# Optimization experiments

Hardware: AMD Instinct MI355X
Metric: run time of the kernel (lower is better)

The kernel has to match this reference:

```python
import jax, jax.numpy as jnp
import numpy as np

B, N, D, K = 16, 512, 256, 12  # batch, nodes, node_dim, num edge types (4 arg + 4 arg' + punct +/- + no_edges +/-)
ITERATION_STEPS = 1


def setup_inputs() -> dict:
    key = jax.random.key(0)
    ks = jax.random.split(key, 8)
    node = jax.random.normal(ks[0], (B, N, D), dtype=jnp.float32)
    node_mask = jax.random.randint(ks[1], (B, N), 0, 2, dtype=jnp.int32)
    graphs = jax.random.randint(ks[2], (K, B, N, N), 0, 2, dtype=jnp.int32)
    s = 1.0 / np.sqrt(D)
    Ww = jax.random.normal(ks[3], (1, D), dtype=jnp.float32) * s   # _node_weight_fc
    bw = jnp.zeros((1,), dtype=jnp.float32)
    Ws = jax.random.normal(ks[4], (D, D), dtype=jnp.float32) * s   # _self_node_fc
    bs = jnp.zeros((D,), dtype=jnp.float32)
    Wk = jax.random.normal(ks[5], (K, D, D), dtype=jnp.float32) * s  # 12 bias-free per-edge-type linears
    return {"node": node, "Ww": Ww, "bw": bw, "Ws": Ws, "bs": bs, "Wk": Wk,
            "node_mask": node_mask, "graphs": graphs}


def reference(node, Ww, bw, Ws, bs, Wk, node_mask, graphs):
    dt = node.dtype
    mask = node_mask.astype(dt)
    eye = jnp.eye(N, dtype=dt)
    # dd_graph = mask_row * mask_col * (1 - diag)
    dd = mask[:, None, :] * mask[:, :, None] * (1.0 - eye)          # [B,N,N]
    g = dd[None] * graphs.astype(dt)                                # [K,B,N,N] masked adjacencies
    neigh = g.sum(axis=(0, 3))                                      # [B,N] total neighbor count
    neigh = jnp.where(neigh >= 1, neigh, jnp.ones((), dt))

    all_w = []
    for _ in range(ITERATION_STEPS):
        # (1) node relatedness
        w = jax.nn.sigmoid(node @ Ww.T + bw)[..., 0]                # [B,N]
        all_w.append(w)
        self_info = node @ Ws.T + bs                                # [B,N,D]
        # (2) message propagation for all 12 edge types, batched
        trans = jnp.einsum('bnd,ked->kbne', node, Wk)               # [K,B,N,D] per-type linear (x @ W.T)
        wg = w[None, :, None, :] * g                                # [K,B,N,N] masked node weights
        agg = jnp.einsum('kbmn,kbnd->bmd', wg, trans) / neigh[..., None]
        # (3) update
        node = jax.nn.relu(self_info + agg)

    all_weight = jnp.stack(all_w, axis=1)                           # [B,steps,N]
    return node, all_weight
```

## Files before the change

### kernel.cpp

```cpp
#include <hip/hip_runtime.h>
#include <hip/hip_bf16.h>
#include <math.h>

#define BB 16
#define NN 512
#define DD 256
#define KK 12

typedef __bf16 bf16x8 __attribute__((ext_vector_type(8)));
typedef __bf16 bf16x4 __attribute__((ext_vector_type(4)));
typedef float  f32x4  __attribute__((ext_vector_type(4)));

#define WS_WM     0
#define WS_MASKBF 32768
#define WS_NODEBF 49152
#define WS_NODET  4243456
#define WS_WKBF   8437760
#define WS_WSBF   10010624

__global__ __launch_bounds__(256) void k1_prep(const float* __restrict__ node,
        const float* __restrict__ Ww, const float* __restrict__ bw,
        const int* __restrict__ node_mask,
        float* __restrict__ wm, __bf16* __restrict__ maskbf,
        __bf16* __restrict__ node_bf, float* __restrict__ all_w) {
    int t = threadIdx.x;
    int lane = t & 63;
    int row = blockIdx.x * 4 + (t >> 6);
    const float4 nv = *(const float4*)(node + (size_t)row * DD + lane * 4);
    const float4 wv = *(const float4*)(Ww + lane * 4);
    float dot = nv.x*wv.x + nv.y*wv.y + nv.z*wv.z + nv.w*wv.w;
    #pragma unroll
    for (int off = 32; off > 0; off >>= 1) dot += __shfl_xor(dot, off);
    float w = 1.0f / (1.0f + expf(-(dot + bw[0])));
    int mk = node_mask[row];
    if (lane == 0) {
        wm[row]     = w * (float)mk;
        all_w[row]  = w;
        maskbf[row] = (__bf16)(float)mk;
    }
    bf16x4 nb = {(__bf16)nv.x, (__bf16)nv.y, (__bf16)nv.z, (__bf16)nv.w};
    *(bf16x4*)(node_bf + (size_t)row * DD + lane * 4) = nb;
}

__global__ __launch_bounds__(256) void k1b_convert(const float* __restrict__ Wk,
        const float* __restrict__ Ws, __bf16* __restrict__ Wk_bf, __bf16* __restrict__ Ws_bf) {
    const int KDD = KK * DD * DD;
    int idx = (blockIdx.x * 256 + threadIdx.x) * 4;
    if (idx < KDD) {
        float4 v = *(const float4*)(Wk + idx);
        bf16x4 o = {(__bf16)v.x, (__bf16)v.y, (__bf16)v.z, (__bf16)v.w};
        *(bf16x4*)(Wk_bf + idx) = o;
    } else {
        int j = idx - KDD;
        if (j < DD * DD) {
            float4 v = *(const float4*)(Ws + j);
            bf16x4 o = {(__bf16)v.x, (__bf16)v.y, (__bf16)v.z, (__bf16)v.w};
            *(bf16x4*)(Ws_bf + j) = o;
        }
    }
}

__global__ __launch_bounds__(256) void k2_transpose(const float* __restrict__ node,
        const float* __restrict__ wm, __bf16* __restrict__ dst) {
    __shared__ float tile[64][65];
    int bx = blockIdx.x;
    int b = bx >> 5; int rest = bx & 31; int nt = rest >> 2; int dt = rest & 3;
    int n0 = nt * 64, d0 = dt * 64;
    int t = threadIdx.x;
    #pragma unroll
    for (int i = 0; i < 16; i++) {
        int idx = i * 256 + t;
        int n = idx >> 6, d = idx & 63;
        tile[n][d] = node[((size_t)(b * NN + n0 + n)) * DD + d0 + d];
    }
    __syncthreads();
    #pragma unroll
    for (int i = 0; i < 16; i++) {
        int idx = i * 256 + t;
        int d = idx >> 6, n = idx & 63;
        float w = wm[b * NN + n0 + n];
        dst[((size_t)(b * DD + d0 + d)) * NN + n0 + n] = (__bf16)(tile[n][d] * w);
    }
}

__global__ __launch_bounds__(512, 2) void k45_fused(const int* __restrict__ graphs,
        const int* __restrict__ node_mask, const __bf16* __restrict__ maskbf,
        const __bf16* __restrict__ node_t, const __bf16* __restrict__ node_bf,
        const __bf16* __restrict__ Wk_bf, const __bf16* __restrict__ Ws_bf,
        const float* __restrict__ bs, float* __restrict__ out) {
    __shared__ __align__(16) __bf16 Abf[32][520];
    __shared__ __align__(16) __bf16 Tk[32][264];
    __shared__ float cntp[8][32];
    __shared__ float sm[32];
    int bx = blockIdx.x;
    int b  = (bx & 7) + 8 * ((bx >> 3) & 1);
    int mt = bx >> 4;
    int m0 = mt * 32;
    int t = threadIdx.x;
    int lane = t & 63;
    int w = t >> 6;
    int q = lane >> 4;
    int l16 = lane & 15;
    int esub = w * 32;
    int dsub = w * 32;

    int crow = t >> 7;
    int ccol = (t & 127) * 4;

    f32x4 accO[2][2];
    #pragma unroll
    for (int i = 0; i < 2; i++)
        #pragma unroll
        for (int j = 0; j < 2; j++) accO[i][j] = (f32x4){0.f, 0.f, 0.f, 0.f};
    f32x4 accC[2];
    accC[0] = (f32x4){0.f, 0.f, 0.f, 0.f};
    accC[1] = (f32x4){0.f, 0.f, 0.f, 0.f};

    int4 g[8];
    {
        const int4* gb = (const int4*)(graphs + ((size_t)(b * NN + m0)) * NN);
        #pragma unroll
        for (int u = 0; u < 8; u++) g[u] = gb[u * 512 + t];
    }

    #pragma unroll 1
    for (int k = 0; k < KK; k++) {
        #pragma unroll
        for (int u = 0; u < 8; u++) {
            int row = u * 4 + crow;
            unsigned p0 = (unsigned)g[u].x | ((unsigned)g[u].y << 16);
            unsigned p1 = (unsigned)g[u].z | ((unsigned)g[u].w << 16);
            unsigned drel = (unsigned)(m0 + row - ccol);
            if (drel < 2u)      p0 &= ~(0xFFFFu << (16 * drel));
            else if (drel < 4u) p1 &= ~(0xFFFFu << (16 * (drel - 2)));
            uint2 st; st.x = p0 * 0x3F80u; st.y = p1 * 0x3F80u;
            *(uint2*)&Abf[row][ccol] = st;
        }
        __syncthreads();

        if (k < KK - 1) {
            const int4* gb = (const int4*)(graphs + ((size_t)(((k + 1) * BB + b) * NN + m0)) * NN);
            #pragma unroll
            for (int u = 0; u < 8; u++) g[u] = gb[u * 512 + t];
        }

        f32x4 accT[2][2];
        #pragma unroll
        for (int i = 0; i < 2; i++)
            #pragma unroll
            for (int j = 0; j < 2; j++) accT[i][j] = (f32x4){0.f, 0.f, 0.f, 0.f};
        #pragma unroll
        for (int kk = 0; kk < 16; kk++) {
            int n0c = kk * 32;
            bf16x8 af[2], bfr[2];
            #pragma unroll
            for (int fm = 0; fm < 2; fm++)
                af[fm] = *(const bf16x8*)&Abf[fm * 16 + l16][n0c + q * 8];
            #pragma unroll
            for (int fd = 0; fd < 2; fd++)
                bfr[fd] = *(const bf16x8*)(node_t +
                    ((size_t)(b * DD + esub + fd * 16 + l16)) * NN + n0c + q * 8);
            #pragma unroll
            for (int fm = 0; fm < 2; fm++)
                #pragma unroll
                for (int fd = 0; fd < 2; fd++)
                    accT[fm][fd] = __builtin_amdgcn_mfma_f32_16x16x32_bf16(
                        af[fm], bfr[fd], accT[fm][fd], 0, 0, 0);
            if ((kk >> 1) == w) {
                bf16x8 bfm = (bf16x8){0,0,0,0,0,0,0,0};
                if (l16 == 0)
                    bfm = *(const bf16x8*)(maskbf + b * NN + n0c + q * 8);
                accC[0] = __builtin_amdgcn_mfma_f32_16x16x32_bf16(af[0], bfm, accC[0], 0, 0, 0);
                accC[1] = __builtin_amdgcn_mfma_f32_16x16x32_bf16(af[1], bfm, accC[1], 0, 0, 0);
            }
        }
        #pragma unroll
        for (int fm = 0; fm < 2; fm++)
            #pragma unroll
            for (int fd = 0; fd < 2; fd++) {
                int col = esub + fd * 16 + l16;
                #pragma unroll
                for (int r = 0; r < 4; r++)
                    Tk[fm * 16 + q * 4 + r][col] = (__bf16)accT[fm][fd][r];
            }
        __syncthreads();

        #pragma unroll
        for (int ee = 0; ee < 8; ee++) {
            int e0c = ee * 32;
            bf16x8 afT[2], bw2[2];
            #pragma unroll
            for (int fm = 0; fm < 2; fm++)
                afT[fm] = *(const bf16x8*)&Tk[fm * 16 + l16][e0c + q * 8];
            #pragma unroll
            for (int fd = 0; fd < 2; fd++)
                bw2[fd] = *(const bf16x8*)(Wk_bf +
                    ((size_t)(k * DD + dsub + fd * 16 + l16)) * DD + e0c + q * 8);
            #pragma unroll
            for (int fm = 0; fm < 2; fm++)
                #pragma unroll
                for (int fd = 0; fd < 2; fd++)
                    accO[fm][fd] = __builtin_amdgcn_mfma_f32_16x16x32_bf16(
                        afT[fm], bw2[fd], accO[fm][fd], 0, 0, 0);
        }
    }

    if (l16 == 0) {
        #pragma unroll
        for (int fm = 0; fm < 2; fm++)
            #pragma unroll
            for (int r = 0; r < 4; r++)
                cntp[w][fm * 16 + q * 4 + r] = accC[fm][r];
    }
    __syncthreads();
    if (t < 32) {
        float c = 0.0f;
        #pragma unroll
        for (int w8 = 0; w8 < 8; w8++) c += cntp[w8][t];
        int mk = node_mask[b * NN + m0 + t];
        sm[t] = (float)mk / (c >= 0.5f ? c : 1.0f);
    }
    __syncthreads();

    #pragma unroll
    for (int fm = 0; fm < 2; fm++)
        #pragma unroll
        for (int r = 0; r < 4; r++) {
            float s = sm[fm * 16 + q * 4 + r];
            #pragma unroll
            for (int fd = 0; fd < 2; fd++) accO[fm][fd][r] *= s;
        }

    #pragma unroll
    for (int ee = 0; ee < 8; ee++) {
        int e0c = ee * 32;
        bf16x8 afS[2], bwS[2];
        #pragma unroll
        for (int fm = 0; fm < 2; fm++)
            afS[fm] = *(const bf16x8*)(node_bf +
                ((size_t)(b * NN + m0 + fm * 16 + l16)) * DD + e0c + q * 8);
        #pragma unroll
        for (int fd = 0; fd < 2; fd++)
            bwS[fd] = *(const bf16x8*)(Ws_bf +
                ((size_t)(dsub + fd * 16 + l16)) * DD + e0c + q * 8);
        #pragma unroll
        for (int fm = 0; fm < 2; fm++)
            #pragma unroll
            for (int fd = 0; fd < 2; fd++)
                accO[fm][fd] = __builtin_amdgcn_mfma_f32_16x16x32_bf16(
                    afS[fm], bwS[fd], accO[fm][fd], 0, 0, 0);
    }

    #pragma unroll
    for (int fm = 0; fm < 2; fm++)
        #pragma unroll
        for (int fd = 0; fd < 2; fd++) {
            int d = dsub + fd * 16 + l16;
            float bsv = bs[d];
            #pragma unroll
            for (int r = 0; r < 4; r++) {
                int m = m0 + fm * 16 + q * 4 + r;
                float v = accO[fm][fd][r] + bsv;
                out[((size_t)(b * NN + m)) * DD + d] = fmaxf(v, 0.0f);
            }
        }
}

extern "C" void kernel_launch(void* const* d_in, const int* in_sizes, int n_in,
                              void* d_out, int out_size, void* d_ws, size_t ws_size,
                              hipStream_t stream) {
    const float* node      = (const float*)d_in[0];
    const float* Ww        = (const float*)d_in[1];
    const float* bw        = (const float*)d_in[2];
    const float* Ws        = (const float*)d_in[3];
    const float* bs        = (const float*)d_in[4];
    const float* Wk        = (const float*)d_in[5];
    const int*   node_mask = (const int*)d_in[6];
    const int*   graphs    = (const int*)d_in[7];
    float* out   = (float*)d_out;
    float* all_w = out + (size_t)BB * NN * DD;

    char* ws = (char*)d_ws;
    float*  wm      = (float*)(ws + WS_WM);
    __bf16* maskbf  = (__bf16*)(ws + WS_MASKBF);
    __bf16* node_bf = (__bf16*)(ws + WS_NODEBF);
    __bf16* node_t  = (__bf16*)(ws + WS_NODET);
    __bf16* Wk_bf   = (__bf16*)(ws + WS_WKBF);
    __bf16* Ws_bf   = (__bf16*)(ws + WS_WSBF);

    k1_prep    <<<2048, 256, 0, stream>>>(node, Ww, bw, node_mask, wm, maskbf, node_bf, all_w);
    k1b_convert<<< 832, 256, 0, stream>>>(Wk, Ws, Wk_bf, Ws_bf);
    k2_transpose<<<512, 256, 0, stream>>>(node, wm, node_t);
    k45_fused  <<< 256, 512, 0, stream>>>(graphs, node_mask, maskbf, node_t, node_bf,
                                          Wk_bf, Ws_bf, bs, out);
}
```

Measured before the change: 354.8 us.

## Split fused graph kernel into 16-row tiles with halved output columns per block

The fused aggregation kernel changes from 256 blocks of 512 threads, each handling 32 rows, to 1024 blocks of 256 threads. Each block now handles 16 rows and half of the output feature dimension. The intent is to spread work over more blocks and waves per CU to raise occupancy and hide latency. The cost is that each pair of blocks recomputes the full adjacency-times-node product and reads the same graph tiles twice, adding redundant MFMA work and memory traffic.

```diff
diff --git a/kernel.cpp b/kernel.cpp
--- a/kernel.cpp
+++ b/kernel.cpp
@@ -83,51 +83,48 @@
     }
 }
 
-__global__ __launch_bounds__(512, 2) void k45_fused(const int* __restrict__ graphs,
+__global__ __launch_bounds__(256, 4) void k45_fused(const int* __restrict__ graphs,
         const int* __restrict__ node_mask, const __bf16* __restrict__ maskbf,
         const __bf16* __restrict__ node_t, const __bf16* __restrict__ node_bf,
         const __bf16* __restrict__ Wk_bf, const __bf16* __restrict__ Ws_bf,
         const float* __restrict__ bs, float* __restrict__ out) {
-    __shared__ __align__(16) __bf16 Abf[32][520];
-    __shared__ __align__(16) __bf16 Tk[32][264];
-    __shared__ float cntp[8][32];
-    __shared__ float sm[32];
+    __shared__ __align__(16) __bf16 Abf[16][520];
+    __shared__ __align__(16) __bf16 Tk[16][264];
+    __shared__ float cntp[4][16];
+    __shared__ float sm[16];
     int bx = blockIdx.x;
     int b  = (bx & 7) + 8 * ((bx >> 3) & 1);
-    int mt = bx >> 4;
-    int m0 = mt * 32;
+    int dh = (bx >> 4) & 1;
+    int mt = bx >> 5;
+    int m0 = mt * 16;
     int t = threadIdx.x;
     int lane = t & 63;
     int w = t >> 6;
     int q = lane >> 4;
     int l16 = lane & 15;
-    int esub = w * 32;
-    int dsub = w * 32;
-
-    int crow = t >> 7;
-    int ccol = (t & 127) * 4;
-
-    f32x4 accO[2][2];
-    #pragma unroll
-    for (int i = 0; i < 2; i++)
-        #pragma unroll
-        for (int j = 0; j < 2; j++) accO[i][j] = (f32x4){0.f, 0.f, 0.f, 0.f};
-    f32x4 accC[2];
-    accC[0] = (f32x4){0.f, 0.f, 0.f, 0.f};
-    accC[1] = (f32x4){0.f, 0.f, 0.f, 0.f};
+    int esub = w * 64;
+    int dsub = dh * 128 + w * 32;
+
+    int rowpar = t >> 7;
+    int ccol   = (t & 127) * 4;
+
+    f32x4 accO[2];
+    accO[0] = (f32x4){0.f, 0.f, 0.f, 0.f};
+    accO[1] = (f32x4){0.f, 0.f, 0.f, 0.f};
+    f32x4 accC = (f32x4){0.f, 0.f, 0.f, 0.f};
 
     int4 g[8];
     {
         const int4* gb = (const int4*)(graphs + ((size_t)(b * NN + m0)) * NN);
         #pragma unroll
-        for (int u = 0; u < 8; u++) g[u] = gb[u * 512 + t];
+        for (int u = 0; u < 8; u++) g[u] = gb[u * 256 + t];
     }
 
     #pragma unroll 1
     for (int k = 0; k < KK; k++) {
         #pragma unroll
         for (int u = 0; u < 8; u++) {
-            int row = u * 4 + crow;
+            int row = u * 2 + rowpar;
             unsigned p0 = (unsigned)g[u].x | ((unsigned)g[u].y << 16);
             unsigned p1 = (unsigned)g[u].z | ((unsigned)g[u].w << 16);
             unsigned drel = (unsigned)(m0 + row - ccol);
@@ -141,129 +138,100 @@
         if (k < KK - 1) {
             const int4* gb = (const int4*)(graphs + ((size_t)(((k + 1) * BB + b) * NN + m0)) * NN);
             #pragma unroll
-            for (int u = 0; u < 8; u++) g[u] = gb[u * 512 + t];
-        }
-
-        f32x4 accT[2][2];
-        #pragma unroll
-        for (int i = 0; i < 2; i++)
-            #pragma unroll
-            for (int j = 0; j < 2; j++) accT[i][j] = (f32x4){0.f, 0.f, 0.f, 0.f};
+            for (int u = 0; u < 8; u++) g[u] = gb[u * 256 + t];
+        }
+
+        f32x4 accT[4];
+        #pragma unroll
+        for (int i = 0; i < 4; i++) accT[i] = (f32x4){0.f, 0.f, 0.f, 0.f};
         #pragma unroll
         for (int kk = 0; kk < 16; kk++) {
             int n0c = kk * 32;
-            bf16x8 af[2], bfr[2];
-            #pragma unroll
-            for (int fm = 0; fm < 2; fm++)
-                af[fm] = *(const bf16x8*)&Abf[fm * 16 + l16][n0c + q * 8];
-            #pragma unroll
-            for (int fd = 0; fd < 2; fd++)
+            bf16x8 af = *(const bf16x8*)&Abf[l16][n0c + q * 8];
+            bf16x8 bfr[4];
+            #pragma unroll
+            for (int fd = 0; fd < 4; fd++)
                 bfr[fd] = *(const bf16x8*)(node_t +
                     ((size_t)(b * DD + esub + fd * 16 + l16)) * NN + n0c + q * 8);
             #pragma unroll
-            for (int fm = 0; fm < 2; fm++)
-                #pragma unroll
-                for (int fd = 0; fd < 2; fd++)
-                    accT[fm][fd] = __builtin_amdgcn_mfma_f32_16x16x32_bf16(
-                        af[fm], bfr[fd], accT[fm][fd], 0, 0, 0);
-            if ((kk >> 1) == w) {
+            for (int fd = 0; fd < 4; fd++)
+                accT[fd] = __builtin_amdgcn_mfma_f32_16x16x32_bf16(af, bfr[fd], accT[fd], 0, 0, 0);
+            if ((kk >> 2) == w) {
                 bf16x8 bfm = (bf16x8){0,0,0,0,0,0,0,0};
                 if (l16 == 0)
                     bfm = *(const bf16x8*)(maskbf + b * NN + n0c + q * 8);
-                accC[0] = __builtin_amdgcn_mfma_f32_16x16x32_bf16(af[0], bfm, accC[0], 0, 0, 0);
-                accC[1] = __builtin_amdgcn_mfma_f32_16x16x32_bf16(af[1], bfm, accC[1], 0, 0, 0);
+                accC = __builtin_amdgcn_mfma_f32_16x16x32_bf16(af, bfm, accC, 0, 0, 0);
             }
         }
         #pragma unroll
-        for (int fm = 0; fm < 2; fm++)
-            #pragma unroll
-            for (int fd = 0; fd < 2; fd++) {
-                int col = esub + fd * 16 + l16;
-                #pragma unroll
-                for (int r = 0; r < 4; r++)
-                    Tk[fm * 16 + q * 4 + r][col] = (__bf16)accT[fm][fd][r];
-            }
+        for (int fd = 0; fd < 4; fd++) {
+            int col = esub + fd * 16 + l16;
+            #pragma unroll
+            for (int r = 0; r < 4; r++)
+                Tk[q * 4 + r][col] = (__bf16)accT[fd][r];
+        }
         __syncthreads();
 
         #pragma unroll
         for (int ee = 0; ee < 8; ee++) {
             int e0c = ee * 32;
-            bf16x8 afT[2], bw2[2];
-            #pragma unroll
-            for (int fm = 0; fm < 2; fm++)
-                afT[fm] = *(const bf16x8*)&Tk[fm * 16 + l16][e0c + q * 8];
+            bf16x8 afT = *(const bf16x8*)&Tk[l16][e0c + q * 8];
+            bf16x8 bw2[2];
             #pragma unroll
             for (int fd = 0; fd < 2; fd++)
                 bw2[fd] = *(const bf16x8*)(Wk_bf +
                     ((size_t)(k * DD + dsub + fd * 16 + l16)) * DD + e0c + q * 8);
             #pragma unroll
-            for (int fm = 0; fm < 2; fm++)
-                #pragma unroll
-                for (int fd = 0; fd < 2; fd++)
-                    accO[fm][fd] = __builtin_amdgcn_mfma_f32_16x16x32_bf16(
-                        afT[fm], bw2[fd], accO[fm][fd], 0, 0, 0);
+            for (int fd = 0; fd < 2; fd++)
+                accO[fd] = __builtin_amdgcn_mfma_f32_16x16x32_bf16(afT, bw2[fd], accO[fd], 0, 0, 0);
         }
     }
 
     if (l16 == 0) {
         #pragma unroll
-        for (int fm = 0; fm < 2; fm++)
-            #pragma unroll
-            for (int r = 0; r < 4; r++)
-                cntp[w][fm * 16 + q * 4 + r] = accC[fm][r];
+        for (int r = 0; r < 4; r++) cntp[w][q * 4 + r] = accC[r];
     }
     __syncthreads();
-    if (t < 32) {
-        float c = 0.0f;
-        #pragma unroll
-        for (int w8 = 0; w8 < 8; w8++) c += cntp[w8][t];
+    if (t < 16) {
+        float c = cntp[0][t] + cntp[1][t] + cntp[2][t] + cntp[3][t];
         int mk = node_mask[b * NN + m0 + t];
         sm[t] = (float)mk / (c >= 0.5f ? c : 1.0f);
     }
     __syncthreads();
 
     #pragma unroll
-    for (int fm = 0; fm < 2; fm++)
-        #pragma unroll
-        for (int r = 0; r < 4; r++) {
-            float s = sm[fm * 16 + q * 4 + r];
-            #pragma unroll
-            for (int fd = 0; fd < 2; fd++) accO[fm][fd][r] *= s;
-        }
+    for (int r = 0; r < 4; r++) {
+        float s = sm[q * 4 + r];
+        accO[0][r] *= s;
+        accO[1][r] *= s;
+    }
 
     #pragma unroll
     for (int ee = 0; ee < 8; ee++) {
         int e0c = ee * 32;
-        bf16x8 afS[2], bwS[2];
-        #pragma unroll
-        for (int fm = 0; fm < 2; fm++)
-            afS[fm] = *(const bf16x8*)(node_bf +
-                ((size_t)(b * NN + m0 + fm * 16 + l16)) * DD + e0c + q * 8);
+        bf16x8 afS = *(const bf16x8*)(node_bf +
+            ((size_t)(b * NN + m0 + l16)) * DD + e0c + q * 8);
+        bf16x8 bwS[2];
         #pragma unroll
         for (int fd = 0; fd < 2; fd++)
             bwS[fd] = *(const bf16x8*)(Ws_bf +
                 ((size_t)(dsub + fd * 16 + l16)) * DD + e0c + q * 8);
         #pragma unroll
-        for (int fm = 0; fm < 2; fm++)
-            #pragma unroll
-            for (int fd = 0; fd < 2; fd++)
-                accO[fm][fd] = __builtin_amdgcn_mfma_f32_16x16x32_bf16(
-                    afS[fm], bwS[fd], accO[fm][fd], 0, 0, 0);
-    }
-
-    #pragma unroll
-    for (int fm = 0; fm < 2; fm++)
-        #pragma unroll
-        for (int fd = 0; fd < 2; fd++) {
-            int d = dsub + fd * 16 + l16;
-            float bsv = bs[d];
-            #pragma unroll
-            for (int r = 0; r < 4; r++) {
-                int m = m0 + fm * 16 + q * 4 + r;
-                float v = accO[fm][fd][r] + bsv;
-                out[((size_t)(b * NN + m)) * DD + d] = fmaxf(v, 0.0f);
-            }
-        }
+        for (int fd = 0; fd < 2; fd++)
+            accO[fd] = __builtin_amdgcn_mfma_f32_16x16x32_bf16(afS, bwS[fd], accO[fd], 0, 0, 0);
+    }
+
+    #pragma unroll
+    for (int fd = 0; fd < 2; fd++) {
+        int d = dsub + fd * 16 + l16;
+        float bsv = bs[d];
+        #pragma unroll
+        for (int r = 0; r < 4; r++) {
+            int m = m0 + q * 4 + r;
+            float v = accO[fd][r] + bsv;
+            out[((size_t)(b * NN + m)) * DD + d] = fmaxf(v, 0.0f);
+        }
+    }
 }
 
 extern "C" void kernel_launch(void* const* d_in, const int* in_sizes, int n_in,
@@ -291,6 +259,6 @@
     k1_prep    <<<2048, 256, 0, stream>>>(node, Ww, bw, node_mask, wm, maskbf, node_bf, all_w);
     k1b_convert<<< 832, 256, 0, stream>>>(Wk, Ws, Wk_bf, Ws_bf);
     k2_transpose<<<512, 256, 0, stream>>>(node, wm, node_t);
-    k45_fused  <<< 256, 512, 0, stream>>>(graphs, node_mask, maskbf, node_t, node_bf,
+    k45_fused  <<<1024, 256, 0, stream>>>(graphs, node_mask, maskbf, node_t, node_bf,
                                           Wk_bf, Ws_bf, bs, out);
 }
```

New measurement: 928.1 us. 2.62x slower.

## Split edge-type loop across two blocks with partial sums and epilogue kernel

Applied to the files above, without the earlier changes.

The fused kernel's loop over 12 edge types is split into two halves handled by separate blocks, which doubles the grid from 256 to 512 blocks to fill more of the GPU's compute units. Each half writes fp32 partial aggregates to workspace and atomically adds neighbor counts. A new epilogue kernel sums the partials, applies the normalization, and computes the self-node linear plus bias and ReLU. The cost is an extra kernel launch, a memset, and about 16MB of extra global traffic for the partial aggregates.

```diff
diff --git a/kernel.cpp b/kernel.cpp
--- a/kernel.cpp
+++ b/kernel.cpp
@@ -12,11 +12,13 @@
 typedef float  f32x4  __attribute__((ext_vector_type(4)));
 
 #define WS_WM     0
-#define WS_MASKBF 32768
-#define WS_NODEBF 49152
-#define WS_NODET  4243456
-#define WS_WKBF   8437760
-#define WS_WSBF   10010624
+#define WS_NCNT   32768
+#define WS_MASKBF 65536
+#define WS_NODEBF 81920
+#define WS_NODET  4276224
+#define WS_WKBF   8470528
+#define WS_WSBF   10043392
+#define WS_AGG    10174464
 
 __global__ __launch_bounds__(256) void k1_prep(const float* __restrict__ node,
         const float* __restrict__ Ww, const float* __restrict__ bw,
@@ -83,18 +85,16 @@
     }
 }
 
-__global__ __launch_bounds__(512, 2) void k45_fused(const int* __restrict__ graphs,
-        const int* __restrict__ node_mask, const __bf16* __restrict__ maskbf,
-        const __bf16* __restrict__ node_t, const __bf16* __restrict__ node_bf,
-        const __bf16* __restrict__ Wk_bf, const __bf16* __restrict__ Ws_bf,
-        const float* __restrict__ bs, float* __restrict__ out) {
+__global__ __launch_bounds__(512, 2) void k45_partial(const int* __restrict__ graphs,
+        const __bf16* __restrict__ maskbf, const __bf16* __restrict__ node_t,
+        const __bf16* __restrict__ Wk_bf, float* __restrict__ Agg, int* __restrict__ ncnt) {
     __shared__ __align__(16) __bf16 Abf[32][520];
     __shared__ __align__(16) __bf16 Tk[32][264];
     __shared__ float cntp[8][32];
-    __shared__ float sm[32];
     int bx = blockIdx.x;
     int b  = (bx & 7) + 8 * ((bx >> 3) & 1);
-    int mt = bx >> 4;
+    int kh = (bx >> 4) & 1;
+    int mt = bx >> 5;
     int m0 = mt * 32;
     int t = threadIdx.x;
     int lane = t & 63;
@@ -118,13 +118,14 @@
 
     int4 g[8];
     {
-        const int4* gb = (const int4*)(graphs + ((size_t)(b * NN + m0)) * NN);
+        const int4* gb = (const int4*)(graphs + ((size_t)((kh * 6 * BB + b) * NN + m0)) * NN);
         #pragma unroll
         for (int u = 0; u < 8; u++) g[u] = gb[u * 512 + t];
     }
 
     #pragma unroll 1
-    for (int k = 0; k < KK; k++) {
+    for (int kc = 0; kc < 6; kc++) {
+        int k = kh * 6 + kc;
         #pragma unroll
         for (int u = 0; u < 8; u++) {
             int row = u * 4 + crow;
@@ -138,7 +139,7 @@
         }
         __syncthreads();
 
-        if (k < KK - 1) {
+        if (kc < 5) {
             const int4* gb = (const int4*)(graphs + ((size_t)(((k + 1) * BB + b) * NN + m0)) * NN);
             #pragma unroll
             for (int u = 0; u < 8; u++) g[u] = gb[u * 512 + t];
@@ -217,53 +218,78 @@
         float c = 0.0f;
         #pragma unroll
         for (int w8 = 0; w8 < 8; w8++) c += cntp[w8][t];
+        atomicAdd(&ncnt[b * NN + m0 + t], (int)(c + 0.5f));
+    }
+
+    float* Ah = Agg + (size_t)kh * BB * NN * DD;
+    #pragma unroll
+    for (int fm = 0; fm < 2; fm++)
+        #pragma unroll
+        for (int fd = 0; fd < 2; fd++) {
+            int d = dsub + fd * 16 + l16;
+            #pragma unroll
+            for (int r = 0; r < 4; r++) {
+                int m = m0 + fm * 16 + q * 4 + r;
+                Ah[((size_t)(b * NN + m)) * DD + d] = accO[fm][fd][r];
+            }
+        }
+}
+
+__global__ __launch_bounds__(256) void k6_epilogue(const float* __restrict__ Agg,
+        const __bf16* __restrict__ node_bf, const __bf16* __restrict__ Ws_bf,
+        const float* __restrict__ bs, const int* __restrict__ ncnt,
+        const int* __restrict__ node_mask, float* __restrict__ out) {
+    __shared__ float sm[16];
+    int bx = blockIdx.x;
+    int b = bx & 15;
+    int mt = bx >> 4;
+    int m0 = mt * 16;
+    int t = threadIdx.x;
+    int lane = t & 63;
+    int w = t >> 6;
+    int q = lane >> 4;
+    int l16 = lane & 15;
+    int dsub = w * 64;
+
+    if (t < 16) {
+        int c = ncnt[b * NN + m0 + t];
         int mk = node_mask[b * NN + m0 + t];
-        sm[t] = (float)mk / (c >= 0.5f ? c : 1.0f);
-    }
-    __syncthreads();
-
-    #pragma unroll
-    for (int fm = 0; fm < 2; fm++)
-        #pragma unroll
-        for (int r = 0; r < 4; r++) {
-            float s = sm[fm * 16 + q * 4 + r];
-            #pragma unroll
-            for (int fd = 0; fd < 2; fd++) accO[fm][fd][r] *= s;
-        }
-
+        sm[t] = (float)mk / (float)(c >= 1 ? c : 1);
+    }
+
+    f32x4 accS[4];
+    #pragma unroll
+    for (int i = 0; i < 4; i++) accS[i] = (f32x4){0.f, 0.f, 0.f, 0.f};
     #pragma unroll
     for (int ee = 0; ee < 8; ee++) {
         int e0c = ee * 32;
-        bf16x8 afS[2], bwS[2];
-        #pragma unroll
-        for (int fm = 0; fm < 2; fm++)
-            afS[fm] = *(const bf16x8*)(node_bf +
-                ((size_t)(b * NN + m0 + fm * 16 + l16)) * DD + e0c + q * 8);
-        #pragma unroll
-        for (int fd = 0; fd < 2; fd++)
+        bf16x8 afS = *(const bf16x8*)(node_bf +
+            ((size_t)(b * NN + m0 + l16)) * DD + e0c + q * 8);
+        bf16x8 bwS[4];
+        #pragma unroll
+        for (int fd = 0; fd < 4; fd++)
             bwS[fd] = *(const bf16x8*)(Ws_bf +
                 ((size_t)(dsub + fd * 16 + l16)) * DD + e0c + q * 8);
         #pragma unroll
-        for (int fm = 0; fm < 2; fm++)
-            #pragma unroll
-            for (int fd = 0; fd < 2; fd++)
-                accO[fm][fd] = __builtin_amdgcn_mfma_f32_16x16x32_bf16(
-                    afS[fm], bwS[fd], accO[fm][fd], 0, 0, 0);
-    }
-
-    #pragma unroll
-    for (int fm = 0; fm < 2; fm++)
-        #pragma unroll
-        for (int fd = 0; fd < 2; fd++) {
-            int d = dsub + fd * 16 + l16;
-            float bsv = bs[d];
-            #pragma unroll
-            for (int r = 0; r < 4; r++) {
-                int m = m0 + fm * 16 + q * 4 + r;
-                float v = accO[fm][fd][r] + bsv;
-                out[((size_t)(b * NN + m)) * DD + d] = fmaxf(v, 0.0f);
-            }
-        }
+        for (int fd = 0; fd < 4; fd++)
+            accS[fd] = __builtin_amdgcn_mfma_f32_16x16x32_bf16(afS, bwS[fd], accS[fd], 0, 0, 0);
+    }
+    __syncthreads();
+
+    const float* A0 = Agg;
+    const float* A1 = Agg + (size_t)BB * NN * DD;
+    #pragma unroll
+    for (int fd = 0; fd < 4; fd++) {
+        int d = dsub + fd * 16 + l16;
+        float bsv = bs[d];
+        #pragma unroll
+        for (int r = 0; r < 4; r++) {
+            int m = m0 + q * 4 + r;
+            size_t idx = ((size_t)(b * NN + m)) * DD + d;
+            float v = sm[q * 4 + r] * (A0[idx] + A1[idx]) + accS[fd][r] + bsv;
+            out[idx] = fmaxf(v, 0.0f);
+        }
+    }
 }
 
 extern "C" void kernel_launch(void* const* d_in, const int* in_sizes, int n_in,
@@ -282,15 +308,18 @@
 
     char* ws = (char*)d_ws;
     float*  wm      = (float*)(ws + WS_WM);
+    int*    ncnt    = (int*)(ws + WS_NCNT);
     __bf16* maskbf  = (__bf16*)(ws + WS_MASKBF);
     __bf16* node_bf = (__bf16*)(ws + WS_NODEBF);
     __bf16* node_t  = (__bf16*)(ws + WS_NODET);
     __bf16* Wk_bf   = (__bf16*)(ws + WS_WKBF);
     __bf16* Ws_bf   = (__bf16*)(ws + WS_WSBF);
-
+    float*  Agg     = (float*)(ws + WS_AGG);
+
+    hipMemsetAsync(ncnt, 0, BB * NN * sizeof(int), stream);
     k1_prep    <<<2048, 256, 0, stream>>>(node, Ww, bw, node_mask, wm, maskbf, node_bf, all_w);
     k1b_convert<<< 832, 256, 0, stream>>>(Wk, Ws, Wk_bf, Ws_bf);
     k2_transpose<<<512, 256, 0, stream>>>(node, wm, node_t);
-    k45_fused  <<< 256, 512, 0, stream>>>(graphs, node_mask, maskbf, node_t, node_bf,
-                                          Wk_bf, Ws_bf, bs, out);
-}
+    k45_partial<<< 512, 512, 0, stream>>>(graphs, maskbf, node_t, Wk_bf, Agg, ncnt);
+    k6_epilogue<<< 512, 256, 0, stream>>>(Agg, node_bf, Ws_bf, bs, ncnt, node_mask, out);
+}
```

Result: slower. 373.6 us (+5.3%).

## Split fused graph kernel into parallel aggregation and projection stages

Applied to the files above, without the earlier changes.

Replaces the single fused kernel (256 blocks looping over all 12 edge types) with two kernels. Stage A runs one block per (edge type, batch, 64-row tile), computes the masked-adjacency times node product, writes it to a bf16 intermediate buffer, and accumulates neighbor counts with integer atomics instead of extra MFMAs. Stage B reduces over edge types with the per-type weights and adds the self term. The aim is much more parallelism and occupancy, at the cost of a round trip of roughly 50MB of intermediate traffic through global memory plus a memset.

```diff
diff --git a/kernel.cpp b/kernel.cpp
--- a/kernel.cpp
+++ b/kernel.cpp
@@ -12,17 +12,17 @@
 typedef float  f32x4  __attribute__((ext_vector_type(4)));
 
 #define WS_WM     0
-#define WS_MASKBF 32768
-#define WS_NODEBF 49152
-#define WS_NODET  4243456
-#define WS_WKBF   8437760
-#define WS_WSBF   10010624
+#define WS_NCNT   32768
+#define WS_NODEBF 65536
+#define WS_NODET  4259840
+#define WS_WKBF   8454144
+#define WS_WSBF   10027008
+#define WS_T      10158080
 
 __global__ __launch_bounds__(256) void k1_prep(const float* __restrict__ node,
         const float* __restrict__ Ww, const float* __restrict__ bw,
         const int* __restrict__ node_mask,
-        float* __restrict__ wm, __bf16* __restrict__ maskbf,
-        __bf16* __restrict__ node_bf, float* __restrict__ all_w) {
+        float* __restrict__ wm, __bf16* __restrict__ node_bf, float* __restrict__ all_w) {
     int t = threadIdx.x;
     int lane = t & 63;
     int row = blockIdx.x * 4 + (t >> 6);
@@ -34,9 +34,8 @@
     float w = 1.0f / (1.0f + expf(-(dot + bw[0])));
     int mk = node_mask[row];
     if (lane == 0) {
-        wm[row]     = w * (float)mk;
-        all_w[row]  = w;
-        maskbf[row] = (__bf16)(float)mk;
+        wm[row]    = w * (float)mk;
+        all_w[row] = w;
     }
     bf16x4 nb = {(__bf16)nv.x, (__bf16)nv.y, (__bf16)nv.z, (__bf16)nv.w};
     *(bf16x4*)(node_bf + (size_t)row * DD + lane * 4) = nb;
@@ -83,172 +82,217 @@
     }
 }
 
-__global__ __launch_bounds__(512, 2) void k45_fused(const int* __restrict__ graphs,
-        const int* __restrict__ node_mask, const __bf16* __restrict__ maskbf,
-        const __bf16* __restrict__ node_t, const __bf16* __restrict__ node_bf,
-        const __bf16* __restrict__ Wk_bf, const __bf16* __restrict__ Ws_bf,
-        const float* __restrict__ bs, float* __restrict__ out) {
-    __shared__ __align__(16) __bf16 Abf[32][520];
-    __shared__ __align__(16) __bf16 Tk[32][264];
-    __shared__ float cntp[8][32];
+__global__ __launch_bounds__(256) void kA_stageA(const int* __restrict__ graphs,
+        const int* __restrict__ node_mask, const __bf16* __restrict__ node_t,
+        __bf16* __restrict__ T, int* __restrict__ ncnt) {
+    __shared__ __align__(16) __bf16 Asub[64][136];
+    int bx = blockIdx.x;
+    int b  = (bx & 7) + 8 * ((bx >> 3) & 1);
+    int mt = (bx >> 4) & 7;
+    int k  = bx >> 7;
+    int m0 = mt * 64;
+    int t = threadIdx.x;
+    int lane = t & 63;
+    int w = t >> 6;
+    int q = lane >> 4;
+    int l16 = lane & 15;
+    int esub = w * 64;
+
+    f32x4 acc[4][4];
+    #pragma unroll
+    for (int i = 0; i < 4; i++)
+        #pragma unroll
+        for (int j = 0; j < 4; j++) acc[i][j] = (f32x4){0.f, 0.f, 0.f, 0.f};
+
+    int arow = t >> 2;
+    int aq   = t & 3;
+    const int* grow = graphs + ((size_t)((k * BB + b) * NN + m0 + arow)) * NN;
+    const int* mrow = node_mask + b * NN;
+    int mg = m0 + arow;
+    unsigned cnt = 0;
+
+    int4 g[8], mk[8];
+    {
+        int nbase0 = aq * 32;
+        #pragma unroll
+        for (int i = 0; i < 8; i++) g[i]  = *(const int4*)(grow + nbase0 + i * 4);
+        #pragma unroll
+        for (int i = 0; i < 8; i++) mk[i] = *(const int4*)(mrow + nbase0 + i * 4);
+    }
+
+    #pragma unroll 1
+    for (int r0 = 0; r0 < 4; r0++) {
+        int nbase0 = r0 * 128 + aq * 32;
+        #pragma unroll
+        for (int i = 0; i < 8; i++) {
+            int nb = nbase0 + i * 4;
+            unsigned p0 = (unsigned)g[i].x | ((unsigned)g[i].y << 16);
+            unsigned p1 = (unsigned)g[i].z | ((unsigned)g[i].w << 16);
+            unsigned drel = (unsigned)(mg - nb);
+            if (drel < 2u)      p0 &= ~(0xFFFFu << (16 * drel));
+            else if (drel < 4u) p1 &= ~(0xFFFFu << (16 * (drel - 2)));
+            unsigned mp0 = (unsigned)mk[i].x | ((unsigned)mk[i].y << 16);
+            unsigned mp1 = (unsigned)mk[i].z | ((unsigned)mk[i].w << 16);
+            cnt += (p0 & mp0) + (p1 & mp1);
+            uint2 st; st.x = p0 * 0x3F80u; st.y = p1 * 0x3F80u;
+            *(uint2*)&Asub[arow][aq * 32 + i * 4] = st;
+        }
+        __syncthreads();
+
+        if (r0 < 3) {
+            int nb1 = (r0 + 1) * 128 + aq * 32;
+            #pragma unroll
+            for (int i = 0; i < 8; i++) g[i]  = *(const int4*)(grow + nb1 + i * 4);
+            #pragma unroll
+            for (int i = 0; i < 8; i++) mk[i] = *(const int4*)(mrow + nb1 + i * 4);
+        }
+
+        #pragma unroll
+        for (int kk = 0; kk < 4; kk++) {
+            int n0c = r0 * 128 + kk * 32;
+            int lc  = kk * 32;
+            bf16x8 af[4], bfr[4];
+            #pragma unroll
+            for (int fm = 0; fm < 4; fm++)
+                af[fm] = *(const bf16x8*)&Asub[fm * 16 + l16][lc + q * 8];
+            #pragma unroll
+            for (int fd = 0; fd < 4; fd++)
+                bfr[fd] = *(const bf16x8*)(node_t +
+                    ((size_t)(b * DD + esub + fd * 16 + l16)) * NN + n0c + q * 8);
+            #pragma unroll
+            for (int fm = 0; fm < 4; fm++)
+                #pragma unroll
+                for (int fd = 0; fd < 4; fd++)
+                    acc[fm][fd] = __builtin_amdgcn_mfma_f32_16x16x32_bf16(
+                        af[fm], bfr[fd], acc[fm][fd], 0, 0, 0);
+        }
+        __syncthreads();
+    }
+
+    cnt = (cnt & 0xFFFFu) + (cnt >> 16);
+    int ci = (int)cnt;
+    ci += __shfl_xor(ci, 1);
+    ci += __shfl_xor(ci, 2);
+    if (aq == 0) atomicAdd(&ncnt[b * NN + mg], ci);
+
+    #pragma unroll
+    for (int fm = 0; fm < 4; fm++)
+        #pragma unroll
+        for (int fd = 0; fd < 4; fd++) {
+            int col = esub + fd * 16 + l16;
+            #pragma unroll
+            for (int r = 0; r < 4; r++) {
+                int m = m0 + fm * 16 + q * 4 + r;
+                T[((size_t)((b * NN + m) * KK + k)) * DD + col] = (__bf16)acc[fm][fd][r];
+            }
+        }
+}
+
+__global__ __launch_bounds__(256) void kB_stageB(const __bf16* __restrict__ T,
+        const __bf16* __restrict__ Wk_bf, const __bf16* __restrict__ node_bf,
+        const __bf16* __restrict__ Ws_bf, const float* __restrict__ bs,
+        const int* __restrict__ ncnt, const int* __restrict__ node_mask,
+        float* __restrict__ out) {
+    __shared__ __align__(16) __bf16 At[32][264];
     __shared__ float sm[32];
     int bx = blockIdx.x;
     int b  = (bx & 7) + 8 * ((bx >> 3) & 1);
-    int mt = bx >> 4;
+    int mt = (bx >> 4) & 15;
+    int dh = bx >> 8;
     int m0 = mt * 32;
     int t = threadIdx.x;
     int lane = t & 63;
     int w = t >> 6;
     int q = lane >> 4;
     int l16 = lane & 15;
-    int esub = w * 32;
-    int dsub = w * 32;
-
-    int crow = t >> 7;
-    int ccol = (t & 127) * 4;
-
-    f32x4 accO[2][2];
+    int dsub = dh * 128 + w * 32;
+
+    if (t < 32) {
+        int c  = ncnt[b * NN + m0 + t];
+        int mk = node_mask[b * NN + m0 + t];
+        sm[t] = (float)mk / (float)(c >= 1 ? c : 1);
+    }
+
+    f32x4 acc[2][2];
     #pragma unroll
     for (int i = 0; i < 2; i++)
         #pragma unroll
-        for (int j = 0; j < 2; j++) accO[i][j] = (f32x4){0.f, 0.f, 0.f, 0.f};
-    f32x4 accC[2];
-    accC[0] = (f32x4){0.f, 0.f, 0.f, 0.f};
-    accC[1] = (f32x4){0.f, 0.f, 0.f, 0.f};
-
-    int4 g[8];
-    {
-        const int4* gb = (const int4*)(graphs + ((size_t)(b * NN + m0)) * NN);
-        #pragma unroll
-        for (int u = 0; u < 8; u++) g[u] = gb[u * 512 + t];
-    }
+        for (int j = 0; j < 2; j++) acc[i][j] = (f32x4){0.f, 0.f, 0.f, 0.f};
+
+    int srow  = t >> 3;
+    int scol8 = (t & 7) * 8;
 
     #pragma unroll 1
     for (int k = 0; k < KK; k++) {
-        #pragma unroll
-        for (int u = 0; u < 8; u++) {
-            int row = u * 4 + crow;
-            unsigned p0 = (unsigned)g[u].x | ((unsigned)g[u].y << 16);
-            unsigned p1 = (unsigned)g[u].z | ((unsigned)g[u].w << 16);
-            unsigned drel = (unsigned)(m0 + row - ccol);
-            if (drel < 2u)      p0 &= ~(0xFFFFu << (16 * drel));
-            else if (drel < 4u) p1 &= ~(0xFFFFu << (16 * (drel - 2)));
-            uint2 st; st.x = p0 * 0x3F80u; st.y = p1 * 0x3F80u;
-            *(uint2*)&Abf[row][ccol] = st;
-        }
-        __syncthreads();
-
-        if (k < KK - 1) {
-            const int4* gb = (const int4*)(graphs + ((size_t)(((k + 1) * BB + b) * NN + m0)) * NN);
-            #pragma unroll
-            for (int u = 0; u < 8; u++) g[u] = gb[u * 512 + t];
-        }
-
-        f32x4 accT[2][2];
-        #pragma unroll
-        for (int i = 0; i < 2; i++)
-            #pragma unroll
-            for (int j = 0; j < 2; j++) accT[i][j] = (f32x4){0.f, 0.f, 0.f, 0.f};
-        #pragma unroll
-        for (int kk = 0; kk < 16; kk++) {
-            int n0c = kk * 32;
-            bf16x8 af[2], bfr[2];
+        const __bf16* trow = T + ((size_t)((b * NN + m0 + srow) * KK + k)) * DD;
+        bf16x8 a0 = *(const bf16x8*)(trow + scol8);
+        bf16x8 a1 = *(const bf16x8*)(trow + scol8 + 64);
+        bf16x8 a2 = *(const bf16x8*)(trow + scol8 + 128);
+        bf16x8 a3 = *(const bf16x8*)(trow + scol8 + 192);
+        *(bf16x8*)&At[srow][scol8]       = a0;
+        *(bf16x8*)&At[srow][scol8 + 64]  = a1;
+        *(bf16x8*)&At[srow][scol8 + 128] = a2;
+        *(bf16x8*)&At[srow][scol8 + 192] = a3;
+        __syncthreads();
+        #pragma unroll
+        for (int ee = 0; ee < 8; ee++) {
+            int e0c = ee * 32;
+            bf16x8 afT[2], bw2[2];
             #pragma unroll
             for (int fm = 0; fm < 2; fm++)
-                af[fm] = *(const bf16x8*)&Abf[fm * 16 + l16][n0c + q * 8];
+                afT[fm] = *(const bf16x8*)&At[fm * 16 + l16][e0c + q * 8];
             #pragma unroll
             for (int fd = 0; fd < 2; fd++)
-                bfr[fd] = *(const bf16x8*)(node_t +
-                    ((size_t)(b * DD + esub + fd * 16 + l16)) * NN + n0c + q * 8);
+                bw2[fd] = *(const bf16x8*)(Wk_bf +
+                    ((size_t)(k * DD + dsub + fd * 16 + l16)) * DD + e0c + q * 8);
             #pragma unroll
             for (int fm = 0; fm < 2; fm++)
                 #pragma unroll
                 for (int fd = 0; fd < 2; fd++)
-                    accT[fm][fd] = __builtin_amdgcn_mfma_f32_16x16x32_bf16(
-                        af[fm], bfr[fd], accT[fm][fd], 0, 0, 0);
-            if ((kk >> 1) == w) {
-                bf16x8 bfm = (bf16x8){0,0,0,0,0,0,0,0};
-                if (l16 == 0)
-                    bfm = *(const bf16x8*)(maskbf + b * NN + n0c + q * 8);
-                accC[0] = __builtin_amdgcn_mfma_f32_16x16x32_bf16(af[0], bfm, accC[0], 0, 0, 0);
-                accC[1] = __builtin_amdgcn_mfma_f32_16x16x32_bf16(af[1], bfm, accC[1], 0, 0, 0);
-            }
-        }
-        #pragma unroll
-        for (int fm = 0; fm < 2; fm++)
-            #pragma unroll
-            for (int fd = 0; fd < 2; fd++) {
-                int col = esub + fd * 16 + l16;
-                #pragma unroll
-                for (int r = 0; r < 4; r++)
-                    Tk[fm * 16 + q * 4 + r][col] = (__bf16)accT[fm][fd][r];
-            }
-        __syncthreads();
-
+                    acc[fm][fd] = __builtin_amdgcn_mfma_f32_16x16x32_bf16(
+                        afT[fm], bw2[fd], acc[fm][fd], 0, 0, 0);
+        }
+        __syncthreads();
+    }
+
+    #pragma unroll
+    for (int fm = 0; fm < 2; fm++)
+        #pragma unroll
+        for (int r = 0; r < 4; r++) {
+            float s = sm[fm * 16 + q * 4 + r];
+            acc[fm][0][r] *= s;
+            acc[fm][1][r] *= s;
+        }
+
+    {
+        const __bf16* nrow = node_bf + (size_t)(b * NN + m0 + srow) * DD;
+        bf16x8 a0 = *(const bf16x8*)(nrow + scol8);
+        bf16x8 a1 = *(const bf16x8*)(nrow + scol8 + 64);
+        bf16x8 a2 = *(const bf16x8*)(nrow + scol8 + 128);
+        bf16x8 a3 = *(const bf16x8*)(nrow + scol8 + 192);
+        *(bf16x8*)&At[srow][scol8]       = a0;
+        *(bf16x8*)&At[srow][scol8 + 64]  = a1;
+        *(bf16x8*)&At[srow][scol8 + 128] = a2;
+        *(bf16x8*)&At[srow][scol8 + 192] = a3;
+        __syncthreads();
         #pragma unroll
         for (int ee = 0; ee < 8; ee++) {
             int e0c = ee * 32;
-            bf16x8 afT[2], bw2[2];
+            bf16x8 afS[2], bwS[2];
             #pragma unroll
             for (int fm = 0; fm < 2; fm++)
-                afT[fm] = *(const bf16x8*)&Tk[fm * 16 + l16][e0c + q * 8];
+                afS[fm] = *(const bf16x8*)&At[fm * 16 + l16][e0c + q * 8];
             #pragma unroll
             for (int fd = 0; fd < 2; fd++)
-                bw2[fd] = *(const bf16x8*)(Wk_bf +
-                    ((size_t)(k * DD + dsub + fd * 16 + l16)) * DD + e0c + q * 8);
+                bwS[fd] = *(const bf16x8*)(Ws_bf +
+                    ((size_t)(dsub + fd * 16 + l16)) * DD + e0c + q * 8);
             #pragma unroll
             for (int fm = 0; fm < 2; fm++)
                 #pragma unroll
                 for (int fd = 0; fd < 2; fd++)
-                    accO[fm][fd] = __builtin_amdgcn_mfma_f32_16x16x32_bf16(
-                        afT[fm], bw2[fd], accO[fm][fd], 0, 0, 0);
-        }
-    }
-
-    if (l16 == 0) {
-        #pragma unroll
-        for (int fm = 0; fm < 2; fm++)
-            #pragma unroll
-            for (int r = 0; r < 4; r++)
-                cntp[w][fm * 16 + q * 4 + r] = accC[fm][r];
-    }
-    __syncthreads();
-    if (t < 32) {
-        float c = 0.0f;
-        #pragma unroll
-        for (int w8 = 0; w8 < 8; w8++) c += cntp[w8][t];
-        int mk = node_mask[b * NN + m0 + t];
-        sm[t] = (float)mk / (c >= 0.5f ? c : 1.0f);
-    }
-    __syncthreads();
-
-    #pragma unroll
-    for (int fm = 0; fm < 2; fm++)
-        #pragma unroll
-        for (int r = 0; r < 4; r++) {
-            float s = sm[fm * 16 + q * 4 + r];
-            #pragma unroll
-            for (int fd = 0; fd < 2; fd++) accO[fm][fd][r] *= s;
-        }
-
-    #pragma unroll
-    for (int ee = 0; ee < 8; ee++) {
-        int e0c = ee * 32;
-        bf16x8 afS[2], bwS[2];
-        #pragma unroll
-        for (int fm = 0; fm < 2; fm++)
-            afS[fm] = *(const bf16x8*)(node_bf +
-                ((size_t)(b * NN + m0 + fm * 16 + l16)) * DD + e0c + q * 8);
-        #pragma unroll
-        for (int fd = 0; fd < 2; fd++)
-            bwS[fd] = *(const bf16x8*)(Ws_bf +
-                ((size_t)(dsub + fd * 16 + l16)) * DD + e0c + q * 8);
-        #pragma unroll
-        for (int fm = 0; fm < 2; fm++)
-            #pragma unroll
-            for (int fd = 0; fd < 2; fd++)
-                accO[fm][fd] = __builtin_amdgcn_mfma_f32_16x16x32_bf16(
-                    afS[fm], bwS[fd], accO[fm][fd], 0, 0, 0);
+                    acc[fm][fd] = __builtin_amdgcn_mfma_f32_16x16x32_bf16(
+                        afS[fm], bwS[fd], acc[fm][fd], 0, 0, 0);
+        }
     }
 
     #pragma unroll
@@ -260,7 +304,7 @@
             #pragma unroll
             for (int r = 0; r < 4; r++) {
                 int m = m0 + fm * 16 + q * 4 + r;
-                float v = accO[fm][fd][r] + bsv;
+                float v = acc[fm][fd][r] + bsv;
                 out[((size_t)(b * NN + m)) * DD + d] = fmaxf(v, 0.0f);
             }
         }
@@ -282,15 +326,17 @@
 
     char* ws = (char*)d_ws;
     float*  wm      = (float*)(ws + WS_WM);
-    __bf16* maskbf  = (__bf16*)(ws + WS_MASKBF);
+    int*    ncnt    = (int*)(ws + WS_NCNT);
     __bf16* node_bf = (__bf16*)(ws + WS_NODEBF);
     __bf16* node_t  = (__bf16*)(ws + WS_NODET);
     __bf16* Wk_bf   = (__bf16*)(ws + WS_WKBF);
     __bf16* Ws_bf   = (__bf16*)(ws + WS_WSBF);
-
-    k1_prep    <<<2048, 256, 0, stream>>>(node, Ww, bw, node_mask, wm, maskbf, node_bf, all_w);
+    __bf16* Tbuf    = (__bf16*)(ws + WS_T);
+
+    hipMemsetAsync(ncnt, 0, BB * NN * sizeof(int), stream);
+    k1_prep    <<<2048, 256, 0, stream>>>(node, Ww, bw, node_mask, wm, node_bf, all_w);
     k1b_convert<<< 832, 256, 0, stream>>>(Wk, Ws, Wk_bf, Ws_bf);
     k2_transpose<<<512, 256, 0, stream>>>(node, wm, node_t);
-    k45_fused  <<< 256, 512, 0, stream>>>(graphs, node_mask, maskbf, node_t, node_bf,
-                                          Wk_bf, Ws_bf, bs, out);
-}
+    kA_stageA  <<<1536, 256, 0, stream>>>(graphs, node_mask, node_t, Tbuf, ncnt);
+    kB_stageB  <<< 512, 256, 0, stream>>>(Tbuf, Wk_bf, node_bf, Ws_bf, bs, ncnt, node_mask, out);
+}
```

After: 413.2 us. +16.4%, slower.
